# Performance work log

Hardware: AMD Instinct MI355X
Metric: run time of the kernel (lower is better)

## Reference

```python
import jax, jax.numpy as jnp
import numpy as np
from jax.scipy.special import logsumexp

SIGMA = 1.0
EPSILON = 1.0
MAX_ITER = 10


def _gaussian_kernel(x, y, sigma):
    # x: (b, l, d), y: (b, k, d) -> (b, l, k) negative-kernel matrix exp(-||x-y||^2 / (2 sigma^2))
    outer = jnp.einsum('bld,bkd->blk', x, y)
    norm_x = jnp.sum(x * x, axis=2)
    norm_y = jnp.sum(y * y, axis=2)
    dist = (norm_x[:, :, None] + norm_y[:, None, :] - 2.0 * outer) / (2.0 * sigma ** 2)
    return jnp.exp(-jnp.maximum(dist, 0.0))


def setup_inputs() -> dict:
    key = jax.random.key(0)
    kx, ka, ky, kb = jax.random.split(key, 4)
    B, L, K, D = 8, 2048, 2048, 32
    return {
        'x': jax.random.normal(kx, (B, L, D), dtype=jnp.float32),
        'a': jax.random.normal(ka, (B, L), dtype=jnp.float32),
        'y': jax.random.normal(ky, (B, K, D), dtype=jnp.float32),
        'b': jax.random.normal(kb, (B, K), dtype=jnp.float32),
    }


def _sinkhorn_potentials(x, a, y, b):
    sg = jax.lax.stop_gradient
    # Kernel matrices (carry gradient wrt x, y); weights a, b are detached inside kernels.
    Kxx = _gaussian_kernel(x, x, SIGMA) / EPSILON + sg(a)[:, None, :]
    Kyx_base = _gaussian_kernel(y, x, SIGMA)
    Kyx = Kyx_base / EPSILON + sg(a)[:, None, :]
    Kxy = jnp.swapaxes(Kyx_base, 1, 2) / EPSILON + sg(b)[:, None, :]
    Kyy = _gaussian_kernel(y, y, SIGMA) / EPSILON + sg(b)[:, None, :]

    # Sinkhorn loop runs under no_grad in the original: stop-gradient kernels.
    Kxx_s, Kyx_s, Kxy_s, Kyy_s = sg(Kxx), sg(Kyx), sg(Kxy), sg(Kyy)

    def step(carry, _):
        fxx, fyx, fxy, fyy = carry
        # sequential (Gauss-Seidel) update order matches the torch dict order xx, yx, xy, yy
        fxx = 0.5 * fxx - 0.5 * logsumexp(Kxx_s + fxx[:, None, :], axis=2)
        fyx = 0.5 * fyx - 0.5 * logsumexp(Kyx_s + fxy[:, None, :], axis=2)  # uses old fxy
        fxy = 0.5 * fxy - 0.5 * logsumexp(Kxy_s + fyx[:, None, :], axis=2)  # uses new fyx
        fyy = 0.5 * fyy - 0.5 * logsumexp(Kyy_s + fyy[:, None, :], axis=2)
        return (fxx, fyx, fxy, fyy), None

    init = (jnp.zeros_like(a), jnp.zeros_like(b), jnp.zeros_like(a), jnp.zeros_like(b))
    (fxx, fyx, fxy, fyy), _ = jax.lax.scan(step, init, None, length=MAX_ITER)

    # Final differentiable extrapolation step (potentials are detached constants).
    fe_xx = -logsumexp(Kxx + fxx[:, None, :], axis=2)
    fe_yx = -logsumexp(Kyx + fxy[:, None, :], axis=2)
    fe_xy = -logsumexp(Kxy + fyx[:, None, :], axis=2)
    fe_yy = -logsumexp(Kyy + fyy[:, None, :], axis=2)
    f = fe_xy - fe_xx  # (b, l)
    g = fe_yx - fe_yy  # (b, k)
    return f, g


def reference(x, a, y, b):
    f, g = _sinkhorn_potentials(x, a, y, b)
    res = jnp.sum(f * jnp.exp(a), axis=1) + jnp.sum(g * jnp.exp(b), axis=1)
    return res * EPSILON  # (batch,)
```

## Files before the change

### kernel.cpp

```cpp
#include <hip/hip_runtime.h>
#include <hip/hip_bf16.h>

#define B_ 8
#define N_ 2048
#define D_ 32
#define CAP 4096
#define EM1_DIAG 1.7182818284590452f
#define M_   8.0f
#define EM_  2980.9579870417283f

typedef __attribute__((ext_vector_type(8))) short short8;
typedef __attribute__((ext_vector_type(4))) float f32x4;

__global__ void setup_kernel(const float* __restrict__ x, const float* __restrict__ y,
                             unsigned short* __restrict__ xb, unsigned short* __restrict__ yb,
                             float* __restrict__ NX, float* __restrict__ NY,
                             int* __restrict__ cnt)
{
    int t = blockIdx.x * 256 + threadIdx.x;
    const float* src = (t < 16384) ? x : y;
    unsigned short* dstb = (t < 16384) ? xb : yb;
    float* dstn = (t < 16384) ? NX : NY;
    int row = (t < 16384) ? t : (t - 16384);
    const float* p = src + (size_t)row * D_;
    float ss = 0.f;
    unsigned short tmp[D_];
    #pragma unroll
    for (int k = 0; k < D_; k++) {
        float v = p[k];
        ss = fmaf(v, v, ss);
        __hip_bfloat16 h = __float2bfloat16(v);
        tmp[k] = *reinterpret_cast<unsigned short*>(&h);
    }
    #pragma unroll
    for (int k = 0; k < D_; k++) dstb[(size_t)row * D_ + k] = tmp[k];
    dstn[row] = ss * 0.5f;
    if (t < 24) cnt[t] = 0;
}

__global__ __launch_bounds__(256) void discover_kernel(
    const unsigned short* __restrict__ xb, const unsigned short* __restrict__ yb,
    const float* __restrict__ NX, const float* __restrict__ NY,
    int* __restrict__ cnt, uint2* __restrict__ lists)
{
    int m = blockIdx.x >> 8;
    int rem = blockIdx.x & 255;
    int batch = rem >> 5;
    int rowblk = rem & 31;
    const unsigned short* rd = (m == 0) ? xb : yb;
    const float*          rN = (m == 0) ? NX : NY;
    const unsigned short* cd = (m == 1) ? yb : xb;
    const float*          cN = (m == 1) ? NY : NX;

    const int tid = threadIdx.x, lane = tid & 63, wv = tid >> 6;
    const int r0 = rowblk * 64;
    const size_t rowbase = (size_t)batch * N_ + r0;

    short8 afrag[4];
    f32x4 cinit[4];
    #pragma unroll
    for (int g = 0; g < 4; g++) {
        afrag[g] = *reinterpret_cast<const short8*>(
            rd + (rowbase + g * 16 + (lane & 15)) * D_ + (lane >> 4) * 8);
        #pragma unroll
        for (int r = 0; r < 4; r++)
            cinit[g][r] = -rN[rowbase + g * 16 + (lane >> 4) * 4 + r];
    }
    const unsigned short* cdB = cd + (size_t)batch * N_ * D_;
    const float* cNB = cN + batch * N_;
    const int slot = m * 8 + batch;
    uint2* L = lists + (size_t)slot * CAP;

    #pragma unroll 4
    for (int cc = 0; cc < 32; ++cc) {
        int col = wv * 512 + cc * 16 + (lane & 15);
        short8 bfrag = *reinterpret_cast<const short8*>(
            cdB + (size_t)col * D_ + (lane >> 4) * 8);
        float ny = cNB[col];
        f32x4 d[4];
        #pragma unroll
        for (int g = 0; g < 4; g++)
            d[g] = __builtin_amdgcn_mfma_f32_16x16x32_bf16(afrag[g], bfrag, cinit[g], 0, 0, 0);
        float mx = d[0][0];
        #pragma unroll
        for (int g = 0; g < 4; g++)
            #pragma unroll
            for (int r = 0; r < 4; r++) mx = fmaxf(mx, d[g][r]);
        if (__any(mx > ny - 10.0f)) {
            #pragma unroll
            for (int g = 0; g < 4; g++) {
                #pragma unroll
                for (int r = 0; r < 4; r++) {
                    float dist = ny - d[g][r];
                    if (dist < 10.0f) {
                        int i = r0 + g * 16 + (lane >> 4) * 4 + r;
                        if (m == 2 || i != col) {
                            float Gv = __expf(-fmaxf(dist, 0.f));
                            float em1 = __expf(Gv) - 1.0f;
                            int idx = atomicAdd(&cnt[slot], 1);
                            if (idx < CAP)
                                L[idx] = make_uint2(((unsigned)i << 16) | (unsigned)col,
                                                    __float_as_uint(em1));
                        }
                    }
                }
            }
        }
    }
}

__global__ __launch_bounds__(1024) void sinkhorn_kernel(
    const float* __restrict__ a_in, const float* __restrict__ b_in,
    const int* __restrict__ cnt, const uint2* __restrict__ lists,
    float* __restrict__ out)
{
    __shared__ float f[4][N_];
    __shared__ float ew[2][N_];
    __shared__ float ev[4][N_];
    __shared__ float acc[4][N_];
    __shared__ float red2[4][16];
    __shared__ float resacc;

    const int batch = blockIdx.x;
    const int t = threadIdx.x, lane = t & 63, wv = t >> 6;

    const int nxx = min(cnt[0 * 8 + batch], CAP);
    const int nyy = min(cnt[1 * 8 + batch], CAP);
    const int nyx = min(cnt[2 * 8 + batch], CAP);
    const uint2* Lxx = lists + (size_t)(0 * 8 + batch) * CAP;
    const uint2* Lyy = lists + (size_t)(1 * 8 + batch) * CAP;
    const uint2* Lyx = lists + (size_t)(2 * 8 + batch) * CAP;

    uint2 rxx[2], ryy[2], ryx[2];
    #pragma unroll
    for (int q = 0; q < 2; q++) {
        int p = t + 1024 * q;
        rxx[q] = (p < nxx) ? Lxx[p] : make_uint2(0u, 0u);
        ryy[q] = (p < nyy) ? Lyy[p] : make_uint2(0u, 0u);
        ryx[q] = (p < nyx) ? Lyx[p] : make_uint2(0u, 0u);
    }

    #pragma unroll
    for (int q = 0; q < 2; q++) {
        int j = t + 1024 * q;
        ew[0][j] = __expf(a_in[batch * N_ + j] - M_);
        ew[1][j] = __expf(b_in[batch * N_ + j] - M_);
        f[0][j] = 0.f; f[1][j] = 0.f; f[2][j] = 0.f; f[3][j] = 0.f;
    }
    if (t == 0) resacc = 0.f;
    __syncthreads();

    auto stageA = [&]() {
        float ss0 = 0.f, ss1 = 0.f, ss2 = 0.f;
        #pragma unroll
        for (int q = 0; q < 2; q++) {
            int j = t + 1024 * q;
            float e0 = ew[0][j] * __expf(f[0][j]); ev[0][j] = e0; acc[0][j] = e0 * EM1_DIAG; ss0 += e0;
            float e1 = ew[0][j] * __expf(f[2][j]); ev[1][j] = e1; acc[1][j] = 0.f;           ss1 += e1;
            float e2 = ew[1][j] * __expf(f[3][j]); ev[2][j] = e2; acc[2][j] = e2 * EM1_DIAG; ss2 += e2;
        }
        #pragma unroll
        for (int off = 1; off < 64; off <<= 1) {
            ss0 += __shfl_xor(ss0, off, 64);
            ss1 += __shfl_xor(ss1, off, 64);
            ss2 += __shfl_xor(ss2, off, 64);
        }
        if (lane == 0) { red2[0][wv] = ss0; red2[1][wv] = ss1; red2[2][wv] = ss2; }
        __syncthreads();
        float S0 = red2[0][0], S1 = red2[1][0], S2 = red2[2][0];
        #pragma unroll
        for (int k = 1; k < 16; k++) { S0 += red2[0][k]; S1 += red2[1][k]; S2 += red2[2][k]; }
        #pragma unroll
        for (int q = 0; q < 2; q++) {
            int p = t + 1024 * q;
            if (p < nxx) { uint2 e = rxx[q]; atomicAdd(&acc[0][e.x >> 16], ev[0][e.x & 0xFFFFu] * __uint_as_float(e.y)); }
            if (p < nyx) { uint2 e = ryx[q]; atomicAdd(&acc[1][e.x >> 16], ev[1][e.x & 0xFFFFu] * __uint_as_float(e.y)); }
            if (p < nyy) { uint2 e = ryy[q]; atomicAdd(&acc[2][e.x >> 16], ev[2][e.x & 0xFFFFu] * __uint_as_float(e.y)); }
        }
        for (int p = 2048 + t; p < nxx; p += 1024) { uint2 e = Lxx[p]; atomicAdd(&acc[0][e.x >> 16], ev[0][e.x & 0xFFFFu] * __uint_as_float(e.y)); }
        for (int p = 2048 + t; p < nyx; p += 1024) { uint2 e = Lyx[p]; atomicAdd(&acc[1][e.x >> 16], ev[1][e.x & 0xFFFFu] * __uint_as_float(e.y)); }
        for (int p = 2048 + t; p < nyy; p += 1024) { uint2 e = Lyy[p]; atomicAdd(&acc[2][e.x >> 16], ev[2][e.x & 0xFFFFu] * __uint_as_float(e.y)); }
        __syncthreads();
        #pragma unroll
        for (int q = 0; q < 2; q++) {
            int i = t + 1024 * q;
            f[0][i] = 0.5f * f[0][i] - 0.5f * (M_ + __logf(S0 + acc[0][i]));
            f[1][i] = 0.5f * f[1][i] - 0.5f * (M_ + __logf(S1 + acc[1][i]));
            f[3][i] = 0.5f * f[3][i] - 0.5f * (M_ + __logf(S2 + acc[2][i]));
        }
        __syncthreads();
    };

    auto stageB = [&]() {
        float ss0 = 0.f;
        #pragma unroll
        for (int q = 0; q < 2; q++) {
            int j = t + 1024 * q;
            float e0 = ew[1][j] * __expf(f[1][j]); ev[0][j] = e0; acc[0][j] = 0.f; ss0 += e0;
        }
        #pragma unroll
        for (int off = 1; off < 64; off <<= 1) ss0 += __shfl_xor(ss0, off, 64);
        if (lane == 0) red2[0][wv] = ss0;
        __syncthreads();
        float S0 = red2[0][0];
        #pragma unroll
        for (int k = 1; k < 16; k++) S0 += red2[0][k];
        #pragma unroll
        for (int q = 0; q < 2; q++) {
            int p = t + 1024 * q;
            if (p < nyx) { uint2 e = ryx[q]; atomicAdd(&acc[0][e.x & 0xFFFFu], ev[0][e.x >> 16] * __uint_as_float(e.y)); }
        }
        for (int p = 2048 + t; p < nyx; p += 1024) { uint2 e = Lyx[p]; atomicAdd(&acc[0][e.x & 0xFFFFu], ev[0][e.x >> 16] * __uint_as_float(e.y)); }
        __syncthreads();
        #pragma unroll
        for (int q = 0; q < 2; q++) {
            int i = t + 1024 * q;
            f[2][i] = 0.5f * f[2][i] - 0.5f * (M_ + __logf(S0 + acc[0][i]));
        }
        __syncthreads();
    };

    for (int it = 0; it < 10; ++it) { stageA(); stageB(); }

    {
        float ss0 = 0.f, ss1 = 0.f, ss2 = 0.f, ss3 = 0.f;
        #pragma unroll
        for (int q = 0; q < 2; q++) {
            int j = t + 1024 * q;
            float e0 = ew[0][j] * __expf(f[0][j]); ev[0][j] = e0; acc[0][j] = e0 * EM1_DIAG; ss0 += e0;
            float e1 = ew[0][j] * __expf(f[2][j]); ev[1][j] = e1; acc[1][j] = 0.f;           ss1 += e1;
            float e2 = ew[1][j] * __expf(f[1][j]); ev[2][j] = e2; acc[2][j] = 0.f;           ss2 += e2;
            float e3 = ew[1][j] * __expf(f[3][j]); ev[3][j] = e3; acc[3][j] = e3 * EM1_DIAG; ss3 += e3;
        }
        #pragma unroll
        for (int off = 1; off < 64; off <<= 1) {
            ss0 += __shfl_xor(ss0, off, 64);
            ss1 += __shfl_xor(ss1, off, 64);
            ss2 += __shfl_xor(ss2, off, 64);
            ss3 += __shfl_xor(ss3, off, 64);
        }
        if (lane == 0) { red2[0][wv] = ss0; red2[1][wv] = ss1; red2[2][wv] = ss2; red2[3][wv] = ss3; }
        __syncthreads();
        float S0 = red2[0][0], S1 = red2[1][0], S2 = red2[2][0], S3 = red2[3][0];
        #pragma unroll
        for (int k = 1; k < 16; k++) { S0 += red2[0][k]; S1 += red2[1][k]; S2 += red2[2][k]; S3 += red2[3][k]; }
        #pragma unroll
        for (int q = 0; q < 2; q++) {
            int p = t + 1024 * q;
            if (p < nxx) { uint2 e = rxx[q]; atomicAdd(&acc[0][e.x >> 16],    ev[0][e.x & 0xFFFFu] * __uint_as_float(e.y)); }
            if (p < nyx) { uint2 e = ryx[q]; atomicAdd(&acc[1][e.x >> 16],    ev[1][e.x & 0xFFFFu] * __uint_as_float(e.y));
                                             atomicAdd(&acc[2][e.x & 0xFFFFu], ev[2][e.x >> 16]    * __uint_as_float(e.y)); }
            if (p < nyy) { uint2 e = ryy[q]; atomicAdd(&acc[3][e.x >> 16],    ev[3][e.x & 0xFFFFu] * __uint_as_float(e.y)); }
        }
        for (int p = 2048 + t; p < nxx; p += 1024) { uint2 e = Lxx[p]; atomicAdd(&acc[0][e.x >> 16], ev[0][e.x & 0xFFFFu] * __uint_as_float(e.y)); }
        for (int p = 2048 + t; p < nyx; p += 1024) { uint2 e = Lyx[p]; atomicAdd(&acc[1][e.x >> 16], ev[1][e.x & 0xFFFFu] * __uint_as_float(e.y));
                                                     atomicAdd(&acc[2][e.x & 0xFFFFu], ev[2][e.x >> 16] * __uint_as_float(e.y)); }
        for (int p = 2048 + t; p < nyy; p += 1024) { uint2 e = Lyy[p]; atomicAdd(&acc[3][e.x >> 16], ev[3][e.x & 0xFFFFu] * __uint_as_float(e.y)); }
        __syncthreads();
        float ctr = 0.f;
        #pragma unroll
        for (int q = 0; q < 2; q++) {
            int i = t + 1024 * q;
            float r0 = M_ + __logf(S0 + acc[0][i]);
            float r1 = M_ + __logf(S1 + acc[1][i]);
            float r2 = M_ + __logf(S2 + acc[2][i]);
            float r3 = M_ + __logf(S3 + acc[3][i]);
            ctr += (r0 - r2) * ew[0][i] * EM_ + (r3 - r1) * ew[1][i] * EM_;
        }
        #pragma unroll
        for (int off = 1; off < 64; off <<= 1) ctr += __shfl_xor(ctr, off, 64);
        if (lane == 0) atomicAdd(&resacc, ctr);
        __syncthreads();
        if (t == 0) out[batch] = resacc;
    }
}

extern "C" void kernel_launch(void* const* d_in, const int* in_sizes, int n_in,
                              void* d_out, int out_size, void* d_ws, size_t ws_size,
                              hipStream_t stream)
{
    const float* x = (const float*)d_in[0];
    const float* a = (const float*)d_in[1];
    const float* y = (const float*)d_in[2];
    const float* b = (const float*)d_in[3];
    float* out = (float*)d_out;

    char* ws = (char*)d_ws;
    size_t o = 0;
    unsigned short* xb = (unsigned short*)(ws + o); o += (size_t)B_ * N_ * D_ * 2;
    unsigned short* yb = (unsigned short*)(ws + o); o += (size_t)B_ * N_ * D_ * 2;
    float* NX = (float*)(ws + o); o += (size_t)B_ * N_ * 4;
    float* NY = (float*)(ws + o); o += (size_t)B_ * N_ * 4;
    int* cnt = (int*)(ws + o); o += 128;
    uint2* lists = (uint2*)(ws + o); o += (size_t)3 * 8 * CAP * 8;

    setup_kernel<<<128, 256, 0, stream>>>(x, y, xb, yb, NX, NY, cnt);
    discover_kernel<<<3 * 256, 256, 0, stream>>>(xb, yb, NX, NY, cnt, lists);
    sinkhorn_kernel<<<B_, 1024, 0, stream>>>(a, b, cnt, lists, out);
}
```

Baseline: 178.9 us.

## Split discover grid finer, vectorize setup I/O, drop stage barriers, tree-reduce sums

The discover kernel now splits each row block's columns into four chunks, launching four times as many blocks with a shorter, fully unrolled inner loop. The setup kernel uses float4 loads and short8 bf16 stores, and the row-norm loads in discover are vectorized. The Sinkhorn kernel drops the trailing __syncthreads at the end of each stage, relying on same-thread index ownership for the f/ev/acc handoffs, and replaces the serial 16-element shared reductions with a balanced tree. The barrier removal depends on subtle ordering assumptions, and more discover blocks mean more atomic contention on the list counters.

```diff
diff --git a/kernel.cpp b/kernel.cpp
--- a/kernel.cpp
+++ b/kernel.cpp
@@ -22,18 +22,27 @@
     unsigned short* dstb = (t < 16384) ? xb : yb;
     float* dstn = (t < 16384) ? NX : NY;
     int row = (t < 16384) ? t : (t - 16384);
-    const float* p = src + (size_t)row * D_;
+    const float4* p = reinterpret_cast<const float4*>(src + (size_t)row * D_);
     float ss = 0.f;
-    unsigned short tmp[D_];
-    #pragma unroll
-    for (int k = 0; k < D_; k++) {
-        float v = p[k];
-        ss = fmaf(v, v, ss);
-        __hip_bfloat16 h = __float2bfloat16(v);
-        tmp[k] = *reinterpret_cast<unsigned short*>(&h);
-    }
-    #pragma unroll
-    for (int k = 0; k < D_; k++) dstb[(size_t)row * D_ + k] = tmp[k];
+    float4 v[8];
+    #pragma unroll
+    for (int k = 0; k < 8; k++) {
+        v[k] = p[k];
+        ss += v[k].x * v[k].x + v[k].y * v[k].y + v[k].z * v[k].z + v[k].w * v[k].w;
+    }
+    short8* dst8 = reinterpret_cast<short8*>(dstb + (size_t)row * D_);
+    #pragma unroll
+    for (int k = 0; k < 4; k++) {
+        const float fv[8] = { v[2*k].x, v[2*k].y, v[2*k].z, v[2*k].w,
+                              v[2*k+1].x, v[2*k+1].y, v[2*k+1].z, v[2*k+1].w };
+        short8 o;
+        #pragma unroll
+        for (int e = 0; e < 8; e++) {
+            __hip_bfloat16 h = __float2bfloat16(fv[e]);
+            o[e] = *reinterpret_cast<const short*>(&h);
+        }
+        dst8[k] = o;
+    }
     dstn[row] = ss * 0.5f;
     if (t < 24) cnt[t] = 0;
 }
@@ -43,10 +52,12 @@
     const float* __restrict__ NX, const float* __restrict__ NY,
     int* __restrict__ cnt, uint2* __restrict__ lists)
 {
-    int m = blockIdx.x >> 8;
-    int rem = blockIdx.x & 255;
-    int batch = rem >> 5;
-    int rowblk = rem & 31;
+    int m = blockIdx.x >> 10;
+    int rem = blockIdx.x & 1023;
+    int batch = rem >> 7;
+    int rem2 = rem & 127;
+    int rowblk = rem2 >> 2;
+    int cchunk = rem2 & 3;
     const unsigned short* rd = (m == 0) ? xb : yb;
     const float*          rN = (m == 0) ? NX : NY;
     const unsigned short* cd = (m == 1) ? yb : xb;
@@ -62,18 +73,19 @@
     for (int g = 0; g < 4; g++) {
         afrag[g] = *reinterpret_cast<const short8*>(
             rd + (rowbase + g * 16 + (lane & 15)) * D_ + (lane >> 4) * 8);
-        #pragma unroll
-        for (int r = 0; r < 4; r++)
-            cinit[g][r] = -rN[rowbase + g * 16 + (lane >> 4) * 4 + r];
+        float4 nv = *reinterpret_cast<const float4*>(
+            rN + rowbase + g * 16 + (lane >> 4) * 4);
+        cinit[g][0] = -nv.x; cinit[g][1] = -nv.y; cinit[g][2] = -nv.z; cinit[g][3] = -nv.w;
     }
     const unsigned short* cdB = cd + (size_t)batch * N_ * D_;
     const float* cNB = cN + batch * N_;
     const int slot = m * 8 + batch;
     uint2* L = lists + (size_t)slot * CAP;
-
-    #pragma unroll 4
-    for (int cc = 0; cc < 32; ++cc) {
-        int col = wv * 512 + cc * 16 + (lane & 15);
+    const int c0 = cchunk * 512 + wv * 128;
+
+    #pragma unroll
+    for (int cc = 0; cc < 8; ++cc) {
+        int col = c0 + cc * 16 + (lane & 15);
         short8 bfrag = *reinterpret_cast<const short8*>(
             cdB + (size_t)col * D_ + (lane >> 4) * 8);
         float ny = cNB[col];
@@ -81,11 +93,11 @@
         #pragma unroll
         for (int g = 0; g < 4; g++)
             d[g] = __builtin_amdgcn_mfma_f32_16x16x32_bf16(afrag[g], bfrag, cinit[g], 0, 0, 0);
-        float mx = d[0][0];
-        #pragma unroll
-        for (int g = 0; g < 4; g++)
-            #pragma unroll
-            for (int r = 0; r < 4; r++) mx = fmaxf(mx, d[g][r]);
+        float m0 = fmaxf(fmaxf(d[0][0], d[0][1]), fmaxf(d[0][2], d[0][3]));
+        float m1 = fmaxf(fmaxf(d[1][0], d[1][1]), fmaxf(d[1][2], d[1][3]));
+        float m2 = fmaxf(fmaxf(d[2][0], d[2][1]), fmaxf(d[2][2], d[2][3]));
+        float m3 = fmaxf(fmaxf(d[3][0], d[3][1]), fmaxf(d[3][2], d[3][3]));
+        float mx = fmaxf(fmaxf(m0, m1), fmaxf(m2, m3));
         if (__any(mx > ny - 10.0f)) {
             #pragma unroll
             for (int g = 0; g < 4; g++) {
@@ -109,6 +121,11 @@
     }
 }
 
+__device__ __forceinline__ float tree16(const float* r) {
+    return (((r[0] + r[1]) + (r[2] + r[3])) + ((r[4] + r[5]) + (r[6] + r[7])))
+         + (((r[8] + r[9]) + (r[10] + r[11])) + ((r[12] + r[13]) + (r[14] + r[15])));
+}
+
 __global__ __launch_bounds__(1024) void sinkhorn_kernel(
     const float* __restrict__ a_in, const float* __restrict__ b_in,
     const int* __restrict__ cnt, const uint2* __restrict__ lists,
@@ -167,9 +184,7 @@
         }
         if (lane == 0) { red2[0][wv] = ss0; red2[1][wv] = ss1; red2[2][wv] = ss2; }
         __syncthreads();
-        float S0 = red2[0][0], S1 = red2[1][0], S2 = red2[2][0];
-        #pragma unroll
-        for (int k = 1; k < 16; k++) { S0 += red2[0][k]; S1 += red2[1][k]; S2 += red2[2][k]; }
+        float S0 = tree16(red2[0]), S1 = tree16(red2[1]), S2 = tree16(red2[2]);
         #pragma unroll
         for (int q = 0; q < 2; q++) {
             int p = t + 1024 * q;
@@ -188,7 +203,6 @@
             f[1][i] = 0.5f * f[1][i] - 0.5f * (M_ + __logf(S1 + acc[1][i]));
             f[3][i] = 0.5f * f[3][i] - 0.5f * (M_ + __logf(S2 + acc[2][i]));
         }
-        __syncthreads();
     };
 
     auto stageB = [&]() {
@@ -202,9 +216,7 @@
         for (int off = 1; off < 64; off <<= 1) ss0 += __shfl_xor(ss0, off, 64);
         if (lane == 0) red2[0][wv] = ss0;
         __syncthreads();
-        float S0 = red2[0][0];
-        #pragma unroll
-        for (int k = 1; k < 16; k++) S0 += red2[0][k];
+        float S0 = tree16(red2[0]);
         #pragma unroll
         for (int q = 0; q < 2; q++) {
             int p = t + 1024 * q;
@@ -217,7 +229,6 @@
             int i = t + 1024 * q;
             f[2][i] = 0.5f * f[2][i] - 0.5f * (M_ + __logf(S0 + acc[0][i]));
         }
-        __syncthreads();
     };
 
     for (int it = 0; it < 10; ++it) { stageA(); stageB(); }
@@ -241,16 +252,14 @@
         }
         if (lane == 0) { red2[0][wv] = ss0; red2[1][wv] = ss1; red2[2][wv] = ss2; red2[3][wv] = ss3; }
         __syncthreads();
-        float S0 = red2[0][0], S1 = red2[1][0], S2 = red2[2][0], S3 = red2[3][0];
-        #pragma unroll
-        for (int k = 1; k < 16; k++) { S0 += red2[0][k]; S1 += red2[1][k]; S2 += red2[2][k]; S3 += red2[3][k]; }
+        float S0 = tree16(red2[0]), S1 = tree16(red2[1]), S2 = tree16(red2[2]), S3 = tree16(red2[3]);
         #pragma unroll
         for (int q = 0; q < 2; q++) {
             int p = t + 1024 * q;
-            if (p < nxx) { uint2 e = rxx[q]; atomicAdd(&acc[0][e.x >> 16],    ev[0][e.x & 0xFFFFu] * __uint_as_float(e.y)); }
-            if (p < nyx) { uint2 e = ryx[q]; atomicAdd(&acc[1][e.x >> 16],    ev[1][e.x & 0xFFFFu] * __uint_as_float(e.y));
-                                             atomicAdd(&acc[2][e.x & 0xFFFFu], ev[2][e.x >> 16]    * __uint_as_float(e.y)); }
-            if (p < nyy) { uint2 e = ryy[q]; atomicAdd(&acc[3][e.x >> 16],    ev[3][e.x & 0xFFFFu] * __uint_as_float(e.y)); }
+            if (p < nxx) { uint2 e = rxx[q]; atomicAdd(&acc[0][e.x >> 16],      ev[0][e.x & 0xFFFFu] * __uint_as_float(e.y)); }
+            if (p < nyx) { uint2 e = ryx[q]; atomicAdd(&acc[1][e.x >> 16],      ev[1][e.x & 0xFFFFu] * __uint_as_float(e.y));
+                                             atomicAdd(&acc[2][e.x & 0xFFFFu], ev[2][e.x >> 16]      * __uint_as_float(e.y)); }
+            if (p < nyy) { uint2 e = ryy[q]; atomicAdd(&acc[3][e.x >> 16],      ev[3][e.x & 0xFFFFu] * __uint_as_float(e.y)); }
         }
         for (int p = 2048 + t; p < nxx; p += 1024) { uint2 e = Lxx[p]; atomicAdd(&acc[0][e.x >> 16], ev[0][e.x & 0xFFFFu] * __uint_as_float(e.y)); }
         for (int p = 2048 + t; p < nyx; p += 1024) { uint2 e = Lyx[p]; atomicAdd(&acc[1][e.x >> 16], ev[1][e.x & 0xFFFFu] * __uint_as_float(e.y));
@@ -295,6 +304,6 @@
     uint2* lists = (uint2*)(ws + o); o += (size_t)3 * 8 * CAP * 8;
 
     setup_kernel<<<128, 256, 0, stream>>>(x, y, xb, yb, NX, NY, cnt);
-    discover_kernel<<<3 * 256, 256, 0, stream>>>(xb, yb, NX, NY, cnt, lists);
+    discover_kernel<<<3 * 1024, 256, 0, stream>>>(xb, yb, NX, NY, cnt, lists);
     sinkhorn_kernel<<<B_, 1024, 0, stream>>>(a, b, cnt, lists, out);
 }
```

After: 188.0 us. 5.1% more time.
